# Kernel optimization log

Hardware: AMD Instinct MI355X
Metric: run time of the kernel (lower is better)

The kernel has to match this reference:

```python
import jax, jax.numpy as jnp
import numpy as np

HEADS = 8
DIM_HEAD = 32
SCALE = DIM_HEAD ** -0.5
EPS = 1e-12  # F.normalize eps


def _rmsnorm_ch(t, g):
    # F.normalize(t, dim=1) * g * sqrt(C)  (normalize_dim=1)
    c = t.shape[1]
    norm = jnp.sqrt(jnp.sum(t * t, axis=1, keepdims=True))
    return t / jnp.maximum(norm, EPS) * g[None, :, None, None] * (c ** 0.5)


def setup_inputs() -> dict:
    key = jax.random.key(0)
    ks = jax.random.split(key, 4)
    B, C, H, W = 16, 256, 64, 64
    hidden = HEADS * DIM_HEAD  # 256
    x = jax.random.normal(ks[0], (B, C, H, W), dtype=jnp.float32)
    g1 = jnp.ones((C,), dtype=jnp.float32)
    # conv 1x1 weights stored as [out_ch, in_ch]
    w_qkv = jax.random.normal(ks[1], (hidden * 3, C), dtype=jnp.float32) * (1.0 / np.sqrt(C))
    w_out = jax.random.normal(ks[2], (C, hidden), dtype=jnp.float32) * (1.0 / np.sqrt(hidden))
    b_out = jnp.zeros((C,), dtype=jnp.float32)
    g2 = jnp.ones((C,), dtype=jnp.float32)
    return {"x": x, "g1": g1, "w_qkv": w_qkv, "w_out": w_out, "b_out": b_out, "g2": g2}


def reference(x, g1, w_qkv, w_out, b_out, g2):
    b, c, h, w = x.shape
    n = h * w
    xn = _rmsnorm_ch(x, g1)
    # 1x1 conv (no bias) == channel matmul
    qkv = jnp.einsum('oc,bchw->bohw', w_qkv, xn)
    q, k, v = jnp.split(qkv, 3, axis=1)
    # b (h c) x y -> b h c (x y)
    q = q.reshape(b, HEADS, DIM_HEAD, n)
    k = k.reshape(b, HEADS, DIM_HEAD, n)
    v = v.reshape(b, HEADS, DIM_HEAD, n)
    q = jax.nn.softmax(q, axis=-2) * SCALE  # softmax over dim_head
    k = jax.nn.softmax(k, axis=-1)          # softmax over sequence
    context = jnp.einsum('bhdn,bhen->bhde', k, v)  # [b,h,d,e] small
    out = jnp.einsum('bhde,bhdn->bhen', context, q)
    out = out.reshape(b, HEADS * DIM_HEAD, h, w)
    out = jnp.einsum('oc,bchw->bohw', w_out, out) + b_out[None, :, None, None]
    return _rmsnorm_ch(out, g2) + x
```

## Files before the change

### kernel.cpp

```cpp
#include <hip/hip_runtime.h>
#include <math.h>


#define B_ 16
#define C_ 256
#define N_ 4096
#define QKV_ 768
#define SCALE_ 0.17677669529663687f
#define EPS_ 1e-12f

typedef __attribute__((ext_vector_type(8))) short bf16x8;
typedef __attribute__((ext_vector_type(4))) float f32x4;

__device__ __forceinline__ ushort f2bf(float f) {
    union { float f; uint u; } x; x.f = f;
    uint r = (x.u + 0x7FFFu + ((x.u >> 16) & 1u)) >> 16;
    return (ushort)r;
}
__device__ __forceinline__ float bf2f(ushort s) {
    union { uint u; float f; } x; x.u = ((uint)s) << 16;
    return x.f;
}

__global__ __launch_bounds__(256) void k_prep(const float* __restrict__ w_qkv,
                                              const float* __restrict__ g1,
                                              ushort* __restrict__ Wp) {
    int o = blockIdx.x, c = threadIdx.x;
    Wp[(size_t)o * 256 + c] = f2bf(w_qkv[(size_t)o * 256 + c] * g1[c]);
}

__global__ __launch_bounds__(256) void k_rnorm(const float* __restrict__ x,
                                               float* __restrict__ rinv) {
    int p = blockIdx.x * 256 + threadIdx.x;
    int b = p >> 12, n = p & 4095;
    const float* xb = x + (size_t)b * C_ * N_ + n;
    float ss = 0.f;
    #pragma unroll 8
    for (int c = 0; c < 256; ++c) { float v = xb[(size_t)c * N_]; ss += v * v; }
    rinv[p] = 16.f / fmaxf(sqrtf(ss), EPS_);
}

__global__ __launch_bounds__(256) void k_gemm_qkv(const ushort* __restrict__ Wp,
                                                  const float* __restrict__ x,
                                                  const float* __restrict__ rinv,
                                                  ushort* __restrict__ qkv) {
    __shared__ ushort Asub[128][40];
    __shared__ ushort Bsub[128][40];
    const int b = blockIdx.z;
    const int row0 = blockIdx.y * 128;
    const int col0 = blockIdx.x * 128;
    const int t = threadIdx.x;
    const int l = t & 63, w = t >> 6;
    const int wr = w >> 1, wc = w & 1;
    const float* xb = x + (size_t)b * C_ * N_;
    f32x4 acc[4][4] = {};

    for (int k0 = 0; k0 < 256; k0 += 32) {
        {
            int r = t >> 1, ko = (t & 1) * 16;
            const uint4* src = (const uint4*)(Wp + (size_t)(row0 + r) * 256 + k0 + ko);
            *(uint4*)&Asub[r][ko]     = src[0];
            *(uint4*)&Asub[r][ko + 8] = src[1];
        }
        {
            int nl = t & 127, kk0 = (t >> 7) * 16;
            uint pk[8];
            #pragma unroll
            for (int j = 0; j < 8; ++j) {
                ushort lo = f2bf(xb[(size_t)(k0 + kk0 + 2 * j) * N_ + col0 + nl]);
                ushort hi = f2bf(xb[(size_t)(k0 + kk0 + 2 * j + 1) * N_ + col0 + nl]);
                pk[j] = (uint)lo | ((uint)hi << 16);
            }
            *(uint4*)&Bsub[nl][kk0]     = make_uint4(pk[0], pk[1], pk[2], pk[3]);
            *(uint4*)&Bsub[nl][kk0 + 8] = make_uint4(pk[4], pk[5], pk[6], pk[7]);
        }
        __syncthreads();
        bf16x8 af[4], bfv[4];
        #pragma unroll
        for (int m = 0; m < 4; ++m)
            af[m] = *(const bf16x8*)&Asub[wr * 64 + m * 16 + (l & 15)][(l >> 4) * 8];
        #pragma unroll
        for (int n = 0; n < 4; ++n)
            bfv[n] = *(const bf16x8*)&Bsub[wc * 64 + n * 16 + (l & 15)][(l >> 4) * 8];
        #pragma unroll
        for (int m = 0; m < 4; ++m)
            #pragma unroll
            for (int n = 0; n < 4; ++n)
                acc[m][n] = __builtin_amdgcn_mfma_f32_16x16x32_bf16(af[m], bfv[n], acc[m][n], 0, 0, 0);
        __syncthreads();
    }

    ushort* qb = qkv + (size_t)b * QKV_ * N_;
    const float* rv = rinv + (size_t)b * N_;
    const bool isq = (row0 < 256);
    #pragma unroll
    for (int n = 0; n < 4; ++n) {
        int cg = col0 + wc * 64 + n * 16 + (l & 15);
        float rs = rv[cg];
        float f[4][4];
        #pragma unroll
        for (int m = 0; m < 4; ++m)
            #pragma unroll
            for (int r = 0; r < 4; ++r) f[m][r] = acc[m][n][r] * rs;
        if (isq) {
            float mxA = -1e30f, mxB = -1e30f;
            #pragma unroll
            for (int r = 0; r < 4; ++r) {
                mxA = fmaxf(mxA, fmaxf(f[0][r], f[1][r]));
                mxB = fmaxf(mxB, fmaxf(f[2][r], f[3][r]));
            }
            mxA = fmaxf(mxA, __shfl_xor(mxA, 16));
            mxA = fmaxf(mxA, __shfl_xor(mxA, 32));
            mxB = fmaxf(mxB, __shfl_xor(mxB, 16));
            mxB = fmaxf(mxB, __shfl_xor(mxB, 32));
            float sA = 0.f, sB = 0.f;
            #pragma unroll
            for (int r = 0; r < 4; ++r) {
                f[0][r] = __expf(f[0][r] - mxA); sA += f[0][r];
                f[1][r] = __expf(f[1][r] - mxA); sA += f[1][r];
                f[2][r] = __expf(f[2][r] - mxB); sB += f[2][r];
                f[3][r] = __expf(f[3][r] - mxB); sB += f[3][r];
            }
            sA += __shfl_xor(sA, 16); sA += __shfl_xor(sA, 32);
            sB += __shfl_xor(sB, 16); sB += __shfl_xor(sB, 32);
            float iA = 1.f / sA, iB = 1.f / sB;
            #pragma unroll
            for (int r = 0; r < 4; ++r) {
                f[0][r] *= iA; f[1][r] *= iA;
                f[2][r] *= iB; f[3][r] *= iB;
            }
        }
        #pragma unroll
        for (int m = 0; m < 4; ++m) {
            int rbase = row0 + wr * 64 + m * 16 + (l >> 4) * 4;
            #pragma unroll
            for (int r = 0; r < 4; ++r)
                qb[(size_t)(rbase + r) * N_ + cg] = f2bf(f[m][r]);
        }
    }
}

__global__ __launch_bounds__(256) void k_ctxpart(const ushort* __restrict__ qkv,
                                                 float* __restrict__ ctxp,
                                                 float* __restrict__ sums_p) {
    __shared__ float red[4][32][33];
    __shared__ float redp[4][32];
    int bh = blockIdx.x, s = blockIdx.y;
    int b = bh >> 3, h = bh & 7;
    int t = threadIdx.x, l = t & 63, w = t >> 6;
    const ushort* kb = qkv + (size_t)b * QKV_ * N_ + (size_t)(256 + h * 32) * N_;
    const ushort* vb = qkv + (size_t)b * QKV_ * N_ + (size_t)(512 + h * 32) * N_;
    const int n0base = s * 1024 + w * 256;
    const int row = l & 15, grp = l >> 4;
    f32x4 acc[2][2] = {};
    float psA = 0.f, psB = 0.f;

    for (int it = 0; it < 8; ++it) {
        int n0 = n0base + it * 32 + grp * 8;
        bf16x8 k0 = *(const bf16x8*)&kb[(size_t)row * N_ + n0];
        bf16x8 k1 = *(const bf16x8*)&kb[(size_t)(row + 16) * N_ + n0];
        bf16x8 v0 = *(const bf16x8*)&vb[(size_t)row * N_ + n0];
        bf16x8 v1 = *(const bf16x8*)&vb[(size_t)(row + 16) * N_ + n0];
        bf16x8 p0, p1;
        #pragma unroll
        for (int j = 0; j < 8; ++j) {
            ushort r0 = f2bf(__expf(bf2f((ushort)k0[j])));
            ushort r1 = f2bf(__expf(bf2f((ushort)k1[j])));
            p0[j] = (short)r0; p1[j] = (short)r1;
            psA += bf2f(r0); psB += bf2f(r1);
        }
        acc[0][0] = __builtin_amdgcn_mfma_f32_16x16x32_bf16(p0, v0, acc[0][0], 0, 0, 0);
        acc[0][1] = __builtin_amdgcn_mfma_f32_16x16x32_bf16(p0, v1, acc[0][1], 0, 0, 0);
        acc[1][0] = __builtin_amdgcn_mfma_f32_16x16x32_bf16(p1, v0, acc[1][0], 0, 0, 0);
        acc[1][1] = __builtin_amdgcn_mfma_f32_16x16x32_bf16(p1, v1, acc[1][1], 0, 0, 0);
    }

    psA += __shfl_xor(psA, 16); psA += __shfl_xor(psA, 32);
    psB += __shfl_xor(psB, 16); psB += __shfl_xor(psB, 32);
    #pragma unroll
    for (int mi = 0; mi < 2; ++mi)
        #pragma unroll
        for (int ni = 0; ni < 2; ++ni)
            #pragma unroll
            for (int r = 0; r < 4; ++r)
                red[w][mi * 16 + grp * 4 + r][ni * 16 + row] = acc[mi][ni][r];
    if (l < 16) { redp[w][l] = psA; redp[w][16 + l] = psB; }
    __syncthreads();

    size_t base = (size_t)(s * 128 + bh) * 32;
    #pragma unroll
    for (int i = t; i < 1024; i += 256) {
        int d = i >> 5, e = i & 31;
        ctxp[(base + d) * 32 + e] =
            red[0][d][e] + red[1][d][e] + red[2][d][e] + red[3][d][e];
    }
    if (t < 32)
        sums_p[base + t] = redp[0][t] + redp[1][t] + redp[2][t] + redp[3][t];
}

__global__ __launch_bounds__(256) void k_fold(const float* __restrict__ w_out,
                                              const float* __restrict__ ctxp,
                                              const float* __restrict__ sums_p,
                                              ushort* __restrict__ M) {
    __shared__ float cn[32][33];
    __shared__ float sinv[32];
    int bh = blockIdx.x;
    int b = bh >> 3, h = bh & 7;
    int t = threadIdx.x;
    if (t < 32) {
        float st = 0.f;
        #pragma unroll
        for (int s = 0; s < 4; ++s) st += sums_p[(size_t)(s * 128 + bh) * 32 + t];
        sinv[t] = SCALE_ / st;
    }
    #pragma unroll
    for (int i = t; i < 1024; i += 256) {
        int d = i >> 5, e = i & 31;
        float cv = 0.f;
        #pragma unroll
        for (int s = 0; s < 4; ++s)
            cv += ctxp[((size_t)(s * 128 + bh) * 32 + d) * 32 + e];
        cn[e][d] = cv;
    }
    __syncthreads();
    float wreg[32];
    const float* wr = w_out + (size_t)t * 256 + h * 32;
    #pragma unroll
    for (int e = 0; e < 32; e += 4) {
        float4 wv = *(const float4*)&wr[e];
        wreg[e] = wv.x; wreg[e + 1] = wv.y; wreg[e + 2] = wv.z; wreg[e + 3] = wv.w;
    }
    float acc[32] = {};
    #pragma unroll
    for (int e = 0; e < 32; ++e) {
        float we = wreg[e];
        #pragma unroll
        for (int d = 0; d < 32; ++d) acc[d] += we * cn[e][d];
    }
    ushort* Mrow = M + ((size_t)b * 256 + t) * 256 + h * 32;
    #pragma unroll
    for (int d = 0; d < 32; ++d) Mrow[d] = f2bf(acc[d] * sinv[d]);
}

__global__ __launch_bounds__(512) void k_final(const ushort* __restrict__ M,
                                               const ushort* __restrict__ qkv,
                                               const float* __restrict__ b_out,
                                               const float* __restrict__ g2,
                                               const float* __restrict__ x,
                                               float* __restrict__ out) {
    __shared__ ushort Asub[256][40];
    __shared__ ushort Bsub[128][40];
    __shared__ float ss2[4][128];
    int b = blockIdx.y;
    int col0 = blockIdx.x * 128;
    int t = threadIdx.x, l = t & 63, w = t >> 6;
    int wr = w >> 1, wc = w & 1;
    const ushort* Mb = M + (size_t)b * 256 * 256;
    const ushort* qs = qkv + (size_t)b * QKV_ * N_;
    f32x4 acc[4][4] = {};

    for (int k0 = 0; k0 < 256; k0 += 32) {
        {
            int r = t >> 1, ko = (t & 1) * 16;
            const uint4* src = (const uint4*)(Mb + (size_t)r * 256 + k0 + ko);
            *(uint4*)&Asub[r][ko]     = src[0];
            *(uint4*)&Asub[r][ko + 8] = src[1];
        }
        {
            int nl = t & 127, kk0 = (t >> 7) * 8;
            uint pk[4];
            #pragma unroll
            for (int j = 0; j < 4; ++j) {
                ushort lo = qs[(size_t)(k0 + kk0 + 2 * j) * N_ + col0 + nl];
                ushort hi = qs[(size_t)(k0 + kk0 + 2 * j + 1) * N_ + col0 + nl];
                pk[j] = (uint)lo | ((uint)hi << 16);
            }
            *(uint4*)&Bsub[nl][kk0] = make_uint4(pk[0], pk[1], pk[2], pk[3]);
        }
        __syncthreads();
        bf16x8 af[4], bfv[4];
        #pragma unroll
        for (int m = 0; m < 4; ++m)
            af[m] = *(const bf16x8*)&Asub[wr * 64 + m * 16 + (l & 15)][(l >> 4) * 8];
        #pragma unroll
        for (int n = 0; n < 4; ++n)
            bfv[n] = *(const bf16x8*)&Bsub[wc * 64 + n * 16 + (l & 15)][(l >> 4) * 8];
        #pragma unroll
        for (int m = 0; m < 4; ++m)
            #pragma unroll
            for (int n = 0; n < 4; ++n)
                acc[m][n] = __builtin_amdgcn_mfma_f32_16x16x32_bf16(af[m], bfv[n], acc[m][n], 0, 0, 0);
        __syncthreads();
    }

    #pragma unroll
    for (int n = 0; n < 4; ++n) {
        float local = 0.f;
        #pragma unroll
        for (int m = 0; m < 4; ++m) {
            int obase = wr * 64 + m * 16 + (l >> 4) * 4;
            #pragma unroll
            for (int r = 0; r < 4; ++r) {
                float f = acc[m][n][r] + b_out[obase + r];
                acc[m][n][r] = f;
                local += f * f;
            }
        }
        local += __shfl_xor(local, 16);
        local += __shfl_xor(local, 32);
        if ((l >> 4) == 0) ss2[wr][wc * 64 + n * 16 + (l & 15)] = local;
    }
    __syncthreads();
    const float* xb = x + (size_t)b * C_ * N_;
    float* ob = out + (size_t)b * C_ * N_;
    #pragma unroll
    for (int n = 0; n < 4; ++n) {
        int cl = wc * 64 + n * 16 + (l & 15);
        int cg = col0 + cl;
        float tot = ss2[0][cl] + ss2[1][cl] + ss2[2][cl] + ss2[3][cl];
        float rs = 16.f / fmaxf(sqrtf(tot), EPS_);
        #pragma unroll
        for (int m = 0; m < 4; ++m) {
            int obase = wr * 64 + m * 16 + (l >> 4) * 4;
            #pragma unroll
            for (int r = 0; r < 4; ++r) {
                int o = obase + r;
                ob[(size_t)o * N_ + cg] = acc[m][n][r] * rs * g2[o] + xb[(size_t)o * N_ + cg];
            }
        }
    }
}

extern "C" void kernel_launch(void* const* d_in, const int* in_sizes, int n_in,
                              void* d_out, int out_size, void* d_ws, size_t ws_size,
                              hipStream_t stream) {
    const float* x     = (const float*)d_in[0];
    const float* g1    = (const float*)d_in[1];
    const float* w_qkv = (const float*)d_in[2];
    const float* w_out = (const float*)d_in[3];
    const float* b_out = (const float*)d_in[4];
    const float* g2    = (const float*)d_in[5];
    float* out = (float*)d_out;
    char* ws = (char*)d_ws;

    float*  rinv   = (float*)(ws + 0);
    ushort* Wp     = (ushort*)(ws + 262144);
    float*  ctxp   = (float*)(ws + 655360);
    float*  sums_p = (float*)(ws + 2752512);
    ushort* Mm     = (ushort*)(ws + 2818048);
    ushort* qkv    = (ushort*)(ws + 4915200);

    k_prep<<<768, 256, 0, stream>>>(w_qkv, g1, Wp);
    k_rnorm<<<256, 256, 0, stream>>>(x, rinv);
    k_gemm_qkv<<<dim3(32, 6, 16), 256, 0, stream>>>(Wp, x, rinv, qkv);
    k_ctxpart<<<dim3(128, 4), 256, 0, stream>>>(qkv, ctxp, sums_p);
    k_fold<<<128, 256, 0, stream>>>(w_out, ctxp, sums_p, Mm);
    k_final<<<dim3(32, 16), 512, 0, stream>>>(Mm, qkv, b_out, g2, x, out);
}
```

Before: 150.1 us.

## Pre-normalize x to transposed bf16 and split QKV GEMM into KV and Q passes

A new kernel computes the channel RMS norm and writes normalized x as a token-major bf16 tensor, replacing the rinv kernel and the per-tile fp32-to-bf16 conversion of strided x loads inside the GEMM. The QKV GEMM then loads both operands with contiguous vector reads. It runs as two launches: K/V first, and Q (with its softmax) written transposed after ctxpart and fold, reusing the KV buffer so k_final can read Q rows contiguously. This adds an extra 32 MB bf16 intermediate write and read and one more launch, in exchange for coalesced loads and no repeated conversion work.

```diff
diff --git a/kernel.cpp b/kernel.cpp
--- a/kernel.cpp
+++ b/kernel.cpp
@@ -5,7 +5,6 @@
 #define B_ 16
 #define C_ 256
 #define N_ 4096
-#define QKV_ 768
 #define SCALE_ 0.17677669529663687f
 #define EPS_ 1e-12f
 
@@ -29,59 +28,73 @@
     Wp[(size_t)o * 256 + c] = f2bf(w_qkv[(size_t)o * 256 + c] * g1[c]);
 }
 
-__global__ __launch_bounds__(256) void k_rnorm(const float* __restrict__ x,
-                                               float* __restrict__ rinv) {
-    int p = blockIdx.x * 256 + threadIdx.x;
-    int b = p >> 12, n = p & 4095;
-    const float* xb = x + (size_t)b * C_ * N_ + n;
+__global__ __launch_bounds__(256) void k_xconv(const float* __restrict__ x,
+                                               ushort* __restrict__ xnbT) {
+    __shared__ float ssp[4][64];
+    __shared__ float rinv_s[64];
+    __shared__ ushort T[64][268];
+    int b = blockIdx.y, n0 = blockIdx.x * 64;
+    const float* xb = x + (size_t)b * C_ * N_ + n0;
+    int t = threadIdx.x;
+    int nl = t & 63, cg = t >> 6;
     float ss = 0.f;
     #pragma unroll 8
-    for (int c = 0; c < 256; ++c) { float v = xb[(size_t)c * N_]; ss += v * v; }
-    rinv[p] = 16.f / fmaxf(sqrtf(ss), EPS_);
-}
-
-__global__ __launch_bounds__(256) void k_gemm_qkv(const ushort* __restrict__ Wp,
-                                                  const float* __restrict__ x,
-                                                  const float* __restrict__ rinv,
-                                                  ushort* __restrict__ qkv) {
+    for (int i = 0; i < 64; ++i) {
+        float v = xb[(size_t)(cg * 64 + i) * N_ + nl];
+        ss += v * v;
+    }
+    ssp[cg][nl] = ss;
+    __syncthreads();
+    if (t < 64)
+        rinv_s[t] = 16.f / fmaxf(sqrtf(ssp[0][t] + ssp[1][t] + ssp[2][t] + ssp[3][t]), EPS_);
+    __syncthreads();
+    float rv = rinv_s[nl];
+    #pragma unroll 8
+    for (int i = 0; i < 64; ++i) {
+        int c = cg * 64 + i;
+        T[nl][c] = f2bf(xb[(size_t)c * N_ + nl] * rv);
+    }
+    __syncthreads();
+    int j = t >> 2, ch = t & 3;
+    ushort* orow = xnbT + ((size_t)b * N_ + n0 + j) * 256 + ch * 64;
+    #pragma unroll
+    for (int i = 0; i < 8; ++i)
+        *(uint2*)&orow[i * 8] = *(const uint2*)&T[j][ch * 64 + i * 8],
+        *(uint2*)&orow[i * 8 + 4] = *(const uint2*)&T[j][ch * 64 + i * 8 + 4];
+}
+
+__global__ __launch_bounds__(256) void k_gemm(const ushort* __restrict__ Wp,
+                                              const ushort* __restrict__ xnbT,
+                                              ushort* __restrict__ kvOut,
+                                              ushort* __restrict__ qTOut,
+                                              int qmode) {
     __shared__ ushort Asub[128][40];
     __shared__ ushort Bsub[128][40];
     const int b = blockIdx.z;
-    const int row0 = blockIdx.y * 128;
+    const int wrow0 = (qmode ? 0 : 256) + blockIdx.y * 128;
     const int col0 = blockIdx.x * 128;
     const int t = threadIdx.x;
     const int l = t & 63, w = t >> 6;
-    const int wr = w >> 1, wc = w & 1;
-    const float* xb = x + (size_t)b * C_ * N_;
+    const int wr = w >> 1, wc = w & 1, grp = l >> 4;
+    const ushort* xb = xnbT + (size_t)b * N_ * 256;
     f32x4 acc[4][4] = {};
 
     for (int k0 = 0; k0 < 256; k0 += 32) {
-        {
-            int r = t >> 1, ko = (t & 1) * 16;
-            const uint4* src = (const uint4*)(Wp + (size_t)(row0 + r) * 256 + k0 + ko);
-            *(uint4*)&Asub[r][ko]     = src[0];
-            *(uint4*)&Asub[r][ko + 8] = src[1];
-        }
-        {
-            int nl = t & 127, kk0 = (t >> 7) * 16;
-            uint pk[8];
-            #pragma unroll
-            for (int j = 0; j < 8; ++j) {
-                ushort lo = f2bf(xb[(size_t)(k0 + kk0 + 2 * j) * N_ + col0 + nl]);
-                ushort hi = f2bf(xb[(size_t)(k0 + kk0 + 2 * j + 1) * N_ + col0 + nl]);
-                pk[j] = (uint)lo | ((uint)hi << 16);
-            }
-            *(uint4*)&Bsub[nl][kk0]     = make_uint4(pk[0], pk[1], pk[2], pk[3]);
-            *(uint4*)&Bsub[nl][kk0 + 8] = make_uint4(pk[4], pk[5], pk[6], pk[7]);
-        }
+        int r = t >> 1, ko = (t & 1) * 16;
+        const uint4* sa = (const uint4*)(Wp + (size_t)(wrow0 + r) * 256 + k0 + ko);
+        *(uint4*)&Asub[r][ko]     = sa[0];
+        *(uint4*)&Asub[r][ko + 8] = sa[1];
+        const uint4* sb = (const uint4*)(xb + (size_t)(col0 + r) * 256 + k0 + ko);
+        *(uint4*)&Bsub[r][ko]     = sb[0];
+        *(uint4*)&Bsub[r][ko + 8] = sb[1];
         __syncthreads();
         bf16x8 af[4], bfv[4];
         #pragma unroll
         for (int m = 0; m < 4; ++m)
-            af[m] = *(const bf16x8*)&Asub[wr * 64 + m * 16 + (l & 15)][(l >> 4) * 8];
+            af[m] = *(const bf16x8*)&Asub[wr * 64 + m * 16 + (l & 15)][grp * 8];
         #pragma unroll
         for (int n = 0; n < 4; ++n)
-            bfv[n] = *(const bf16x8*)&Bsub[wc * 64 + n * 16 + (l & 15)][(l >> 4) * 8];
+            bfv[n] = *(const bf16x8*)&Bsub[wc * 64 + n * 16 + (l & 15)][grp * 8];
         #pragma unroll
         for (int m = 0; m < 4; ++m)
             #pragma unroll
@@ -90,19 +103,16 @@
         __syncthreads();
     }
 
-    ushort* qb = qkv + (size_t)b * QKV_ * N_;
-    const float* rv = rinv + (size_t)b * N_;
-    const bool isq = (row0 < 256);
-    #pragma unroll
-    for (int n = 0; n < 4; ++n) {
-        int cg = col0 + wc * 64 + n * 16 + (l & 15);
-        float rs = rv[cg];
-        float f[4][4];
-        #pragma unroll
-        for (int m = 0; m < 4; ++m)
-            #pragma unroll
-            for (int r = 0; r < 4; ++r) f[m][r] = acc[m][n][r] * rs;
-        if (isq) {
+    if (qmode) {
+        ushort* qTb = qTOut + (size_t)b * N_ * 256;
+        #pragma unroll
+        for (int n = 0; n < 4; ++n) {
+            int cg = col0 + wc * 64 + n * 16 + (l & 15);
+            float f[4][4];
+            #pragma unroll
+            for (int m = 0; m < 4; ++m)
+                #pragma unroll
+                for (int r = 0; r < 4; ++r) f[m][r] = acc[m][n][r];
             float mxA = -1e30f, mxB = -1e30f;
             #pragma unroll
             for (int r = 0; r < 4; ++r) {
@@ -125,22 +135,32 @@
             sB += __shfl_xor(sB, 16); sB += __shfl_xor(sB, 32);
             float iA = 1.f / sA, iB = 1.f / sB;
             #pragma unroll
-            for (int r = 0; r < 4; ++r) {
-                f[0][r] *= iA; f[1][r] *= iA;
-                f[2][r] *= iB; f[3][r] *= iB;
-            }
-        }
-        #pragma unroll
-        for (int m = 0; m < 4; ++m) {
-            int rbase = row0 + wr * 64 + m * 16 + (l >> 4) * 4;
-            #pragma unroll
-            for (int r = 0; r < 4; ++r)
-                qb[(size_t)(rbase + r) * N_ + cg] = f2bf(f[m][r]);
-        }
-    }
-}
-
-__global__ __launch_bounds__(256) void k_ctxpart(const ushort* __restrict__ qkv,
+            for (int m = 0; m < 4; ++m) {
+                float sc = (m < 2) ? iA : iB;
+                int rbase = wrow0 + wr * 64 + m * 16 + grp * 4;
+                uint2 pk;
+                pk.x = (uint)f2bf(f[m][0] * sc) | ((uint)f2bf(f[m][1] * sc) << 16);
+                pk.y = (uint)f2bf(f[m][2] * sc) | ((uint)f2bf(f[m][3] * sc) << 16);
+                *(uint2*)&qTb[(size_t)cg * 256 + rbase] = pk;
+            }
+        }
+    } else {
+        ushort* kvb = kvOut + (size_t)b * 512 * N_;
+        #pragma unroll
+        for (int n = 0; n < 4; ++n) {
+            int cg = col0 + wc * 64 + n * 16 + (l & 15);
+            #pragma unroll
+            for (int m = 0; m < 4; ++m) {
+                int rbase = wrow0 - 256 + wr * 64 + m * 16 + grp * 4;
+                #pragma unroll
+                for (int r = 0; r < 4; ++r)
+                    kvb[(size_t)(rbase + r) * N_ + cg] = f2bf(acc[m][n][r]);
+            }
+        }
+    }
+}
+
+__global__ __launch_bounds__(256) void k_ctxpart(const ushort* __restrict__ kv,
                                                  float* __restrict__ ctxp,
                                                  float* __restrict__ sums_p) {
     __shared__ float red[4][32][33];
@@ -148,8 +168,8 @@
     int bh = blockIdx.x, s = blockIdx.y;
     int b = bh >> 3, h = bh & 7;
     int t = threadIdx.x, l = t & 63, w = t >> 6;
-    const ushort* kb = qkv + (size_t)b * QKV_ * N_ + (size_t)(256 + h * 32) * N_;
-    const ushort* vb = qkv + (size_t)b * QKV_ * N_ + (size_t)(512 + h * 32) * N_;
+    const ushort* kb = kv + (size_t)b * 512 * N_ + (size_t)(h * 32) * N_;
+    const ushort* vb = kv + (size_t)b * 512 * N_ + (size_t)(256 + h * 32) * N_;
     const int n0base = s * 1024 + w * 256;
     const int row = l & 15, grp = l >> 4;
     f32x4 acc[2][2] = {};
@@ -243,7 +263,7 @@
 }
 
 __global__ __launch_bounds__(512) void k_final(const ushort* __restrict__ M,
-                                               const ushort* __restrict__ qkv,
+                                               const ushort* __restrict__ qT,
                                                const float* __restrict__ b_out,
                                                const float* __restrict__ g2,
                                                const float* __restrict__ x,
@@ -256,7 +276,7 @@
     int t = threadIdx.x, l = t & 63, w = t >> 6;
     int wr = w >> 1, wc = w & 1;
     const ushort* Mb = M + (size_t)b * 256 * 256;
-    const ushort* qs = qkv + (size_t)b * QKV_ * N_;
+    const ushort* qTb = qT + (size_t)b * N_ * 256;
     f32x4 acc[4][4] = {};
 
     for (int k0 = 0; k0 < 256; k0 += 32) {
@@ -267,15 +287,9 @@
             *(uint4*)&Asub[r][ko + 8] = src[1];
         }
         {
-            int nl = t & 127, kk0 = (t >> 7) * 8;
-            uint pk[4];
-            #pragma unroll
-            for (int j = 0; j < 4; ++j) {
-                ushort lo = qs[(size_t)(k0 + kk0 + 2 * j) * N_ + col0 + nl];
-                ushort hi = qs[(size_t)(k0 + kk0 + 2 * j + 1) * N_ + col0 + nl];
-                pk[j] = (uint)lo | ((uint)hi << 16);
-            }
-            *(uint4*)&Bsub[nl][kk0] = make_uint4(pk[0], pk[1], pk[2], pk[3]);
+            int nl = t & 127, ko = (t >> 7) * 8;
+            *(uint4*)&Bsub[nl][ko] =
+                *(const uint4*)(qTb + (size_t)(col0 + nl) * 256 + k0 + ko);
         }
         __syncthreads();
         bf16x8 af[4], bfv[4];
@@ -343,17 +357,19 @@
     float* out = (float*)d_out;
     char* ws = (char*)d_ws;
 
-    float*  rinv   = (float*)(ws + 0);
-    ushort* Wp     = (ushort*)(ws + 262144);
-    float*  ctxp   = (float*)(ws + 655360);
-    float*  sums_p = (float*)(ws + 2752512);
-    ushort* Mm     = (ushort*)(ws + 2818048);
-    ushort* qkv    = (ushort*)(ws + 4915200);
+    ushort* Wp     = (ushort*)(ws + 0);
+    float*  ctxp   = (float*)(ws + 393216);
+    float*  sums_p = (float*)(ws + 2490368);
+    ushort* Mm     = (ushort*)(ws + 2555904);
+    ushort* xnbT   = (ushort*)(ws + 4653056);
+    ushort* kv     = (ushort*)(ws + 38207488);
+    ushort* qT     = kv;
 
     k_prep<<<768, 256, 0, stream>>>(w_qkv, g1, Wp);
-    k_rnorm<<<256, 256, 0, stream>>>(x, rinv);
-    k_gemm_qkv<<<dim3(32, 6, 16), 256, 0, stream>>>(Wp, x, rinv, qkv);
-    k_ctxpart<<<dim3(128, 4), 256, 0, stream>>>(qkv, ctxp, sums_p);
+    k_xconv<<<dim3(64, 16), 256, 0, stream>>>(x, xnbT);
+    k_gemm<<<dim3(32, 4, 16), 256, 0, stream>>>(Wp, xnbT, kv, nullptr, 0);
+    k_ctxpart<<<dim3(128, 4), 256, 0, stream>>>(kv, ctxp, sums_p);
     k_fold<<<128, 256, 0, stream>>>(w_out, ctxp, sums_p, Mm);
-    k_final<<<dim3(32, 16), 512, 0, stream>>>(Mm, qkv, b_out, g2, x, out);
-}
+    k_gemm<<<dim3(32, 2, 16), 256, 0, stream>>>(Wp, xnbT, nullptr, qT, 1);
+    k_final<<<dim3(32, 16), 512, 0, stream>>>(Mm, qT, b_out, g2, x, out);
+}
```

New measurement: 160.7 us (median of 2 runs). +7.1%, slower.
